# Kernel tuning notes

Measured on AMD Instinct MI355X. Metric: run time of the kernel, lower is better.

Reference implementation:

```python
import jax, jax.numpy as jnp
import numpy as np
import math

BS, SEQ, DIM, H, LK = 4, 4096, 768, 12, 256
HD = DIM // H  # 64
WIN = SEQ // LK  # 16, AdaptiveAvgPool1d reduces to uniform windows since SEQ % LK == 0


def setup_inputs() -> dict:
    key = jax.random.key(0)
    ks = jax.random.split(key, 12)
    s = 1.0 / math.sqrt(DIM)
    return {
        "query": jax.random.normal(ks[0], (BS, SEQ, DIM), jnp.float32),
        "key": jax.random.normal(ks[1], (BS, SEQ, DIM), jnp.float32),
        "value": jax.random.normal(ks[2], (BS, SEQ, DIM), jnp.float32),
        "mask": jax.random.normal(ks[3], (BS, SEQ), jnp.float32),  # mask<0 -> padded
        "Wq": jax.random.normal(ks[4], (DIM, DIM), jnp.float32) * s,
        "bq": jnp.zeros((DIM,), jnp.float32),
        "Wk": jax.random.normal(ks[5], (DIM, DIM), jnp.float32) * s,
        "bk": jnp.zeros((DIM,), jnp.float32),
        "Wv": jax.random.normal(ks[6], (DIM, DIM), jnp.float32) * s,
        "bv": jnp.zeros((DIM,), jnp.float32),
        "Wo": jax.random.normal(ks[7], (DIM, DIM), jnp.float32) * s,
        "bo": jnp.zeros((DIM,), jnp.float32),
    }


def reference(query, key, value, mask, Wq, bq, Wk, bk, Wv, bv, Wo, bo):
    bs, q_len, _ = query.shape
    # projections (nn.Linear: x @ W.T + b)
    Q = query @ Wq.T + bq
    K = key @ Wk.T + bk
    V = value @ Wv.T + bv
    # mask-fill padded K/V rows with 0 (mask dim==2 path: bool_mask = mask < 0)
    keep = (mask >= 0)[:, :, None]  # [bs, seq, 1]
    K = jnp.where(keep, K, 0.0)
    V = jnp.where(keep, V, 0.0)
    # adaptive avg pool over sequence -> linformer_k=256 (uniform windows of 16)
    Kc = K.reshape(bs, LK, WIN, DIM).mean(axis=2)  # [bs, 256, dim]
    Vc = V.reshape(bs, LK, WIN, DIM).mean(axis=2)
    # split heads
    Qh = Q.reshape(bs, q_len, H, HD) / math.sqrt(HD)  # scale fused
    Kh = Kc.reshape(bs, LK, H, HD)
    Vh = Vc.reshape(bs, LK, H, HD)
    # low-rank attention: [bs, h, q_len, 256]
    scores = jnp.einsum("bqhd,bkhd->bhqk", Qh, Kh)
    weights = jax.nn.softmax(scores, axis=-1)
    context = jnp.einsum("bhqk,bkhd->bqhd", weights, Vh).reshape(bs, q_len, DIM)
    return context @ Wo.T + bo
```

## Files before the change

kernel.cpp:

```cpp
#include <hip/hip_runtime.h>

#define BS_   4
#define SEQ_  4096
#define DIM_  768
#define NH_   12
#define HD_   64
#define LK_   256

typedef __attribute__((ext_vector_type(8))) short          bf8;
typedef __attribute__((ext_vector_type(8))) unsigned short us8;
typedef __attribute__((ext_vector_type(4))) unsigned short us4;
typedef __attribute__((ext_vector_type(4))) float          f32x4;
typedef __attribute__((ext_vector_type(4))) unsigned int   u32x4;

typedef unsigned int u32g __attribute__((address_space(1)));
typedef unsigned int u32l __attribute__((address_space(3)));

#define LOG2E 1.44269504088896340736f

__device__ __forceinline__ unsigned short f2bf(float f) {
  unsigned u = __builtin_bit_cast(unsigned, f);
  u += 0x7fffu + ((u >> 16) & 1u);
  return (unsigned short)(u >> 16);
}

__device__ __forceinline__ us8 cvt8(const float* __restrict__ p) {
  const float4 a = *(const float4*)p;
  const float4 b = *(const float4*)(p + 4);
  us8 r;
  r[0] = f2bf(a.x); r[1] = f2bf(a.y); r[2] = f2bf(a.z); r[3] = f2bf(a.w);
  r[4] = f2bf(b.x); r[5] = f2bf(b.y); r[6] = f2bf(b.z); r[7] = f2bf(b.w);
  return r;
}

__device__ __forceinline__ f32x4 max4(f32x4 a, f32x4 b) {
  f32x4 r;
  r[0] = fmaxf(a[0], b[0]); r[1] = fmaxf(a[1], b[1]);
  r[2] = fmaxf(a[2], b[2]); r[3] = fmaxf(a[3], b[3]);
  return r;
}

__device__ __forceinline__ float fexp2(float x) {
  float r; asm("v_exp_f32 %0, %1" : "=v"(r) : "v"(x)); return r;
}
__device__ __forceinline__ unsigned cvtpk(float lo, float hi) {
  unsigned r; asm("v_cvt_pk_bf16_f32 %0, %1, %2" : "=v"(r) : "v"(lo), "v"(hi));
  return r;
}

__global__ __launch_bounds__(384) void prep_kernel(
    const float* __restrict__ key, const float* __restrict__ value,
    const float* __restrict__ mask, const float* __restrict__ query,
    const float* __restrict__ Wq, const float* __restrict__ Wk,
    const float* __restrict__ Wv, const float* __restrict__ Wo,
    unsigned short* __restrict__ pk, unsigned short* __restrict__ pv,
    float* __restrict__ frac,
    unsigned short* __restrict__ Qbf, unsigned short* __restrict__ Wbf)
{
  const int bid = blockIdx.x;
  const int tid = threadIdx.x;
  if (bid < 1024) {
    const int b = bid >> 8;
    const int l = bid & 255;
    __shared__ float keep[16];
    __shared__ int   wlist[16];
    __shared__ float wwt[16];
    __shared__ int   nk4s;
    if (tid < 16) keep[tid] = (mask[b * SEQ_ + l * 16 + tid] >= 0.f) ? 1.f : 0.f;
    __syncthreads();
    if (tid == 0) {
      int n = 0; float cnt = 0.f;
      for (int w = 0; w < 16; ++w)
        if (keep[w] != 0.f) { wlist[n] = w; wwt[n] = 1.f; ++n; cnt += 1.f; }
      frac[b * LK_ + l] = cnt * (1.f / 16.f);
      const int n8 = (n + 7) & ~7;
      for (int i = n; i < n8; ++i) { wlist[i] = wlist[0]; wwt[i] = 0.f; }
      if (n == 0) for (int i = 0; i < 8; ++i) { wlist[i] = 0; wwt[i] = 0.f; }
      nk4s = (n == 0) ? 0 : n8;
    }
    __syncthreads();
    const int nk8 = nk4s;
    const int isV = tid >= 192;
    const int c = isV ? tid - 192 : tid;
    const float* src = isV ? value : key;
    const float* base = src + (size_t)(b * SEQ_ + l * 16) * DIM_ + c * 4;
    float4 acc = make_float4(0.f, 0.f, 0.f, 0.f);
    for (int i = 0; i < nk8; i += 8) {
      #pragma unroll
      for (int u = 0; u < 8; ++u) {
        const float4 v = *(const float4*)(base + (size_t)wlist[i + u] * DIM_);
        const float w = wwt[i + u];
        acc.x = fmaf(w, v.x, acc.x); acc.y = fmaf(w, v.y, acc.y);
        acc.z = fmaf(w, v.z, acc.z); acc.w = fmaf(w, v.w, acc.w);
      }
    }
    const float s = 1.f / 16.f;
    unsigned short* dst = isV ? pv : pk;
    us4 o4;
    o4[0] = f2bf(acc.x * s); o4[1] = f2bf(acc.y * s);
    o4[2] = f2bf(acc.z * s); o4[3] = f2bf(acc.w * s);
    *(us4*)(dst + (size_t)(b * LK_ + l) * DIM_ + c * 4) = o4;
    return;
  }
  const int QN8 = (BS_ * SEQ_ * DIM_) / 8;
  const int WN8 = (DIM_ * DIM_) / 8;
  const int i0 = (bid - 1024) * 768 + tid;
  #pragma unroll
  for (int u = 0; u < 2; ++u) {
    const int i = i0 + u * 384;
    if (i < QN8) { *(us8*)(Qbf + (size_t)i * 8) = cvt8(query + (size_t)i * 8); continue; }
    int j = i - QN8;
    const float* src; unsigned short* dst;
    if      (j <     WN8) { src = Wq; dst = Wbf;                   }
    else if (j < 2 * WN8) { src = Wk; dst = Wbf + DIM_*DIM_;     j -=     WN8; }
    else if (j < 3 * WN8) { src = Wv; dst = Wbf + 2*DIM_*DIM_;   j -= 2 * WN8; }
    else if (j < 4 * WN8) { src = Wo; dst = Wbf + 3*DIM_*DIM_;   j -= 3 * WN8; }
    else continue;
    *(us8*)(dst + (size_t)j * 8) = cvt8(src + (size_t)j * 8);
  }
}

template<int MODE, int SWZ>
__global__ __launch_bounds__(256) void gemm_bt(
    const void* __restrict__ Aptr_, const void* __restrict__ Bptr_,
    const float* __restrict__ bias, const float* __restrict__ bias2,
    const float* __restrict__ frac,
    void* __restrict__ Cout, float scale)
{
  constexpr int K  = DIM_;
  constexpr int BK = 64;
  constexpr int NT = K / BK;
  __shared__ __align__(16) unsigned short lA[2][128 * BK];
  __shared__ __align__(16) unsigned short lB[2][128 * BK];
  const int tid  = threadIdx.x;
  const int lane = tid & 63;
  const int wave = tid >> 6;

  int bx, by;
  if (SWZ) {
    const int r = (blockIdx.x & 7) * 96 + (blockIdx.x >> 3);
    bx = r / 6; by = r % 6;
  } else {
    bx = blockIdx.x; by = blockIdx.y;
  }
  const int brow = bx * 128;
  const int bcol = by * 128;

  const unsigned short* A  = (const unsigned short*)Aptr_;
  const unsigned short* Bw = (const unsigned short*)Bptr_;
  const float* bb = bias;
  int isV = 0;
  if (MODE == 34) {
    isV = blockIdx.z;
    A  += (size_t)isV * (BS_ * LK_ * DIM_);
    Bw += (size_t)isV * (DIM_ * DIM_);
    if (isV) bb = bias2;
  }

  const int wr = (wave >> 1) * 64;
  const int wc = (wave & 1) * 64;
  const int fr = lane & 15;
  const int hi = lane >> 4;
  const int rx = fr & 7;

  f32x4 acc[4][4];
  #pragma unroll
  for (int i = 0; i < 4; ++i)
    #pragma unroll
    for (int j = 0; j < 4; ++j) acc[i][j] = (f32x4){0.f, 0.f, 0.f, 0.f};

  const int srow = tid >> 3;
  const int schk = ((tid & 7) ^ (srow & 7)) * 8;

  auto STAGE = [&](int t, int b) {
    const int k0 = t * BK;
    #pragma unroll
    for (int s = 0; s < 4; ++s) {
      __builtin_amdgcn_global_load_lds(
          (const u32g*)(A + (size_t)(brow + srow + s * 32) * K + k0 + schk),
          (u32l*)&lA[b][s * 2048 + tid * 8], 16, 0, 0);
      __builtin_amdgcn_global_load_lds(
          (const u32g*)(Bw + (size_t)(bcol + srow + s * 32) * K + k0 + schk),
          (u32l*)&lB[b][s * 2048 + tid * 8], 16, 0, 0);
    }
  };

  auto COMPUTE = [&](int b) {
    #pragma unroll
    for (int ks = 0; ks < 2; ++ks) {
      bf8 af[4], bfv[4];
      const int c = ks * 4 + hi;
      const int pc = (c ^ rx) * 8;
      #pragma unroll
      for (int mi = 0; mi < 4; ++mi)
        af[mi] = *(const bf8*)&lA[b][(wr + mi * 16 + fr) * BK + pc];
      #pragma unroll
      for (int ni = 0; ni < 4; ++ni)
        bfv[ni] = *(const bf8*)&lB[b][(wc + ni * 16 + fr) * BK + pc];
      #pragma unroll
      for (int mi = 0; mi < 4; ++mi)
        #pragma unroll
        for (int ni = 0; ni < 4; ++ni)
          acc[mi][ni] = __builtin_amdgcn_mfma_f32_16x16x32_bf16(af[mi], bfv[ni], acc[mi][ni], 0, 0, 0);
    }
  };

  STAGE(0, 0);
  STAGE(1, 1);
  asm volatile("s_waitcnt vmcnt(8)" ::: "memory");
  __builtin_amdgcn_s_barrier();

  #pragma unroll 2
  for (int t = 0; t < NT; ++t) {
    COMPUTE(t & 1);
    if (t + 1 < NT) {
      __builtin_amdgcn_s_barrier();
      if (t + 2 < NT) {
        STAGE(t + 2, t & 1);
        asm volatile("s_waitcnt vmcnt(8)" ::: "memory");
      } else {
        asm volatile("s_waitcnt vmcnt(0)" ::: "memory");
      }
      __builtin_amdgcn_s_barrier();
    }
  }

  const int er = (lane >> 4) * 4;
  #pragma unroll
  for (int mi = 0; mi < 4; ++mi) {
    #pragma unroll
    for (int ni = 0; ni < 4; ++ni) {
      #pragma unroll
      for (int j = 0; j < 4; ++j) {
        const int r = brow + wr + mi * 16 + er + j;
        const int c = bcol + wc + ni * 16 + fr;
        float v = acc[mi][ni][j];
        if (MODE == 0) {
          v = (v + bias[c]) * scale;
          ((unsigned short*)Cout)[(size_t)r * DIM_ + c] = f2bf(v);
        } else if (MODE == 2) {
          ((float*)Cout)[(size_t)r * DIM_ + c] = v + bias[c];
        } else {
          v += frac[r] * bb[c];
          const int bb_ = r >> 8, key = r & 255;
          const int hh = c >> 6, dd = c & 63;
          const int bh = bb_ * NH_ + hh;
          size_t idx;
          if (isV) {
            idx = (size_t)bh * 16384 +
                ((key >> 5) * 4 + (dd >> 4)) * 512 + ((key >> 3) & 3) * 128 +
                (dd & 15) * 8 + (key & 7) + 786432;
          } else {
            const int tt = key >> 5, g = (key >> 3) & 3, sub = (key >> 2) & 1, jj = key & 3;
            const int frk = g * 4 + jj;
            idx = (size_t)bh * 16384 +
                (((tt * 2 + sub) * 2) + (dd >> 5)) * 512 + ((dd >> 3) & 3) * 128 +
                frk * 8 + (dd & 7);
          }
          ((unsigned short*)Cout)[idx] = f2bf(v);
        }
      }
    }
  }
}

__global__ __launch_bounds__(512, 4) void attn_fused(
    const unsigned short* __restrict__ Qh,
    const unsigned short* __restrict__ Kf,
    const unsigned short* __restrict__ Vf,
    unsigned short* __restrict__ ctx)
{
  __shared__ __align__(16) unsigned short Ks[16384];
  const int tid  = threadIdx.x;
  const int lane = tid & 63;
  const int wave = tid >> 6;
  const int bh = blockIdx.y;
  const int b = bh / NH_, h = bh % NH_;
  const int fr = lane & 15;
  const int hi = lane >> 4;
  const int qrow = blockIdx.x * 128 + wave * 16;

  {
    const unsigned short* kg = Kf + (size_t)bh * 16384 + tid * 8;
    #pragma unroll
    for (int i = 0; i < 4; ++i)
      __builtin_amdgcn_global_load_lds((const u32g*)(kg + i * 4096),
                                       (u32l*)&Ks[i * 4096 + tid * 8], 16, 0, 0);
  }

  const unsigned short* qp = Qh + (size_t)(b * SEQ_ + qrow + fr) * DIM_ + h * HD_ + hi * 8;
  const bf8 q0 = *(const bf8*)qp;
  const bf8 q1 = *(const bf8*)(qp + 32);

  __syncthreads();

  f32x4 scA[8], scB[8];
  __builtin_amdgcn_s_setprio(1);
  #pragma unroll
  for (int s = 0; s < 8; ++s) {
    const bf8 ka0 = *(const bf8*)&Ks[(s * 4 + 0) * 512 + lane * 8];
    const bf8 ka1 = *(const bf8*)&Ks[(s * 4 + 1) * 512 + lane * 8];
    const bf8 kb0 = *(const bf8*)&Ks[(s * 4 + 2) * 512 + lane * 8];
    const bf8 kb1 = *(const bf8*)&Ks[(s * 4 + 3) * 512 + lane * 8];
    f32x4 x = (f32x4){0.f, 0.f, 0.f, 0.f};
    x = __builtin_amdgcn_mfma_f32_16x16x32_bf16(ka0, q0, x, 0, 0, 0);
    x = __builtin_amdgcn_mfma_f32_16x16x32_bf16(ka1, q1, x, 0, 0, 0);
    scA[s] = x;
    f32x4 y = (f32x4){0.f, 0.f, 0.f, 0.f};
    y = __builtin_amdgcn_mfma_f32_16x16x32_bf16(kb0, q0, y, 0, 0, 0);
    y = __builtin_amdgcn_mfma_f32_16x16x32_bf16(kb1, q1, y, 0, 0, 0);
    scB[s] = y;
  }
  __builtin_amdgcn_s_setprio(0);

  f32x4 tm[8];
  #pragma unroll
  for (int s = 0; s < 8; ++s) tm[s] = max4(scA[s], scB[s]);
  tm[0] = max4(tm[0], tm[4]); tm[1] = max4(tm[1], tm[5]);
  tm[2] = max4(tm[2], tm[6]); tm[3] = max4(tm[3], tm[7]);
  tm[0] = max4(tm[0], tm[2]); tm[1] = max4(tm[1], tm[3]);
  tm[0] = max4(tm[0], tm[1]);
  float m = fmaxf(fmaxf(tm[0][0], tm[0][1]), fmaxf(tm[0][2], tm[0][3]));
  m = fmaxf(m, __shfl_xor(m, 16));
  m = fmaxf(m, __shfl_xor(m, 32));

  f32x4 uA = (f32x4){0.f, 0.f, 0.f, 0.f};
  f32x4 uB = (f32x4){0.f, 0.f, 0.f, 0.f};
  #pragma unroll
  for (int s = 0; s < 8; ++s) {
    #pragma unroll
    for (int j = 0; j < 4; ++j) {
      scA[s][j] = fexp2(scA[s][j] - m);
      scB[s][j] = fexp2(scB[s][j] - m);
    }
    uA += scA[s];
    uB += scB[s];
  }
  const f32x4 uv = uA + uB;
  float sum = (uv[0] + uv[1]) + (uv[2] + uv[3]);
  sum += __shfl_xor(sum, 16);
  sum += __shfl_xor(sum, 32);
  const float inv = 1.f / sum;

  bf8 pa[8];
  #pragma unroll
  for (int s = 0; s < 8; ++s) {
    u32x4 w;
    w[0] = cvtpk(scA[s][0] * inv, scA[s][1] * inv);
    w[1] = cvtpk(scA[s][2] * inv, scA[s][3] * inv);
    w[2] = cvtpk(scB[s][0] * inv, scB[s][1] * inv);
    w[3] = cvtpk(scB[s][2] * inv, scB[s][3] * inv);
    pa[s] = __builtin_bit_cast(bf8, w);
  }

  const unsigned short* vb = Vf + (size_t)bh * 16384 + lane * 8;
  f32x4 acc[4];
  #pragma unroll
  for (int ct = 0; ct < 4; ++ct) acc[ct] = (f32x4){0.f, 0.f, 0.f, 0.f};
  __builtin_amdgcn_s_setprio(1);
  #pragma unroll
  for (int s = 0; s < 8; ++s) {
    #pragma unroll
    for (int ct = 0; ct < 4; ++ct) {
      const bf8 vf = *(const bf8*)(vb + (s * 4 + ct) * 512);
      acc[ct] = __builtin_amdgcn_mfma_f32_16x16x32_bf16(pa[s], vf, acc[ct], 0, 0, 0);
    }
  }
  __builtin_amdgcn_s_setprio(0);

  #pragma unroll
  for (int ct = 0; ct < 4; ++ct)
    #pragma unroll
    for (int j = 0; j < 4; ++j)
      ctx[(size_t)(b * SEQ_ + qrow + hi * 4 + j) * DIM_ + h * HD_ + ct * 16 + fr] =
          f2bf(acc[ct][j]);
}

extern "C" void kernel_launch(void* const* d_in, const int* in_sizes, int n_in,
                              void* d_out, int out_size, void* d_ws, size_t ws_size,
                              hipStream_t stream) {
  const float* query = (const float*)d_in[0];
  const float* key   = (const float*)d_in[1];
  const float* value = (const float*)d_in[2];
  const float* mask  = (const float*)d_in[3];
  const float* Wq    = (const float*)d_in[4];
  const float* bq    = (const float*)d_in[5];
  const float* Wk    = (const float*)d_in[6];
  const float* bk    = (const float*)d_in[7];
  const float* Wv    = (const float*)d_in[8];
  const float* bv    = (const float*)d_in[9];
  const float* Wo    = (const float*)d_in[10];
  const float* bo    = (const float*)d_in[11];
  float* out = (float*)d_out;

  char* ws = (char*)d_ws;
  unsigned short* Qh  = (unsigned short*)ws;
  unsigned short* ctx = (unsigned short*)(ws + 25165824);
  unsigned short* pK  = (unsigned short*)(ws + 50331648);
  unsigned short* pV  = (unsigned short*)(ws + 51904512);
  unsigned short* Kf  = (unsigned short*)(ws + 53477376);
  unsigned short* Vf  = (unsigned short*)(ws + 55050240);
  float*          frac = (float*)(ws + 56623104);
  unsigned short* Wbf = (unsigned short*)(ws + 56627200);
  unsigned short* Qbf = ctx;

  const float qscale = 0.125f * LOG2E;

  prep_kernel<<<dim3(3456), dim3(384), 0, stream>>>(
      key, value, mask, query, Wq, Wk, Wv, Wo, pK, pV, frac, Qbf, Wbf);
  gemm_bt<0, 1><<<dim3(768), dim3(256), 0, stream>>>(
      Qbf, Wbf, bq, nullptr, nullptr, Qh, qscale);
  gemm_bt<34, 0><<<dim3(8, 6, 2), dim3(256), 0, stream>>>(
      pK, Wbf + DIM_*DIM_, bk, bv, frac, Kf, 1.f);
  attn_fused<<<dim3(32, 48), dim3(512), 0, stream>>>(Qh, Kf, Vf, ctx);
  gemm_bt<2, 1><<<dim3(768), dim3(256), 0, stream>>>(
      ctx, Wbf + 3*DIM_*DIM_, bo, nullptr, nullptr, out, 1.f);
}
```

Measured before the change: 127.2 us.

## Fuse fp32-to-bf16 query conversion into the Q projection GEMM

Removes the separate pass in the prep kernel that converted the full fp32 query tensor to bf16 and wrote it to the workspace. A new GEMM kernel loads fp32 query tiles straight into LDS and converts them to bf16 in registers just before the MFMA, using a 64x128 tile. This cuts one full read and write of the query activation tensor, but doubles the A-tile LDS footprint and adds conversion instructions to the GEMM inner loop, with smaller tiles and more blocks.

```diff
diff --git a/kernel.cpp b/kernel.cpp
--- a/kernel.cpp
+++ b/kernel.cpp
@@ -50,12 +50,11 @@
 
 __global__ __launch_bounds__(384) void prep_kernel(
     const float* __restrict__ key, const float* __restrict__ value,
-    const float* __restrict__ mask, const float* __restrict__ query,
+    const float* __restrict__ mask,
     const float* __restrict__ Wq, const float* __restrict__ Wk,
     const float* __restrict__ Wv, const float* __restrict__ Wo,
     unsigned short* __restrict__ pk, unsigned short* __restrict__ pv,
-    float* __restrict__ frac,
-    unsigned short* __restrict__ Qbf, unsigned short* __restrict__ Wbf)
+    float* __restrict__ frac, unsigned short* __restrict__ Wbf)
 {
   const int bid = blockIdx.x;
   const int tid = threadIdx.x;
@@ -102,14 +101,11 @@
     *(us4*)(dst + (size_t)(b * LK_ + l) * DIM_ + c * 4) = o4;
     return;
   }
-  const int QN8 = (BS_ * SEQ_ * DIM_) / 8;
   const int WN8 = (DIM_ * DIM_) / 8;
-  const int i0 = (bid - 1024) * 768 + tid;
-  #pragma unroll
-  for (int u = 0; u < 2; ++u) {
-    const int i = i0 + u * 384;
-    if (i < QN8) { *(us8*)(Qbf + (size_t)i * 8) = cvt8(query + (size_t)i * 8); continue; }
-    int j = i - QN8;
+  const int i0 = (bid - 1024) * 1536 + tid;
+  #pragma unroll
+  for (int u = 0; u < 4; ++u) {
+    int j = i0 + u * 384;
     const float* src; unsigned short* dst;
     if      (j <     WN8) { src = Wq; dst = Wbf;                   }
     else if (j < 2 * WN8) { src = Wk; dst = Wbf + DIM_*DIM_;     j -=     WN8; }
@@ -118,6 +114,117 @@
     else continue;
     *(us8*)(dst + (size_t)j * 8) = cvt8(src + (size_t)j * 8);
   }
+}
+
+__global__ __launch_bounds__(256) void gemm_qf32(
+    const float* __restrict__ Af, const unsigned short* __restrict__ Bw,
+    const float* __restrict__ bias, unsigned short* __restrict__ Cout,
+    float scale)
+{
+  constexpr int K  = DIM_;
+  constexpr int BK = 64;
+  constexpr int NT = K / BK;
+  __shared__ __align__(16) float          lA[2][64 * BK];
+  __shared__ __align__(16) unsigned short lB[2][128 * BK];
+  const int tid  = threadIdx.x;
+  const int lane = tid & 63;
+  const int wave = tid >> 6;
+
+  const int r = (blockIdx.x & 7) * 192 + (blockIdx.x >> 3);
+  const int brow = (r / 6) * 64;
+  const int bcol = (r % 6) * 128;
+
+  const int wr = (wave >> 1) * 32;
+  const int wc = (wave & 1) * 64;
+  const int fr = lane & 15;
+  const int hi = lane >> 4;
+  const int rx = fr & 7;
+
+  f32x4 acc[2][4];
+  #pragma unroll
+  for (int i = 0; i < 2; ++i)
+    #pragma unroll
+    for (int j = 0; j < 4; ++j) acc[i][j] = (f32x4){0.f, 0.f, 0.f, 0.f};
+
+  const int srowB = tid >> 3;
+  const int schkB = ((tid & 7) ^ (srowB & 7)) * 8;
+  const int srowA = tid >> 4;
+  const int posA  = tid & 15;
+  const int csA   = ((posA >> 1) ^ (srowA & 7)) * 8 + (posA & 1) * 4;
+
+  auto STAGE = [&](int t, int b) {
+    const int k0 = t * BK;
+    #pragma unroll
+    for (int s = 0; s < 4; ++s) {
+      __builtin_amdgcn_global_load_lds(
+          (const u32g*)(Af + (size_t)(brow + s * 16 + srowA) * K + k0 + csA),
+          (u32l*)&lA[b][s * 1024 + tid * 4], 16, 0, 0);
+      __builtin_amdgcn_global_load_lds(
+          (const u32g*)(Bw + (size_t)(bcol + s * 32 + srowB) * K + k0 + schkB),
+          (u32l*)&lB[b][s * 2048 + tid * 8], 16, 0, 0);
+    }
+  };
+
+  auto COMPUTE = [&](int b) {
+    #pragma unroll
+    for (int ks = 0; ks < 2; ++ks) {
+      const int c  = ks * 4 + hi;
+      const int pc = c ^ rx;
+      bf8 af[2], bfv[4];
+      #pragma unroll
+      for (int mi = 0; mi < 2; ++mi) {
+        const int ro = (wr + mi * 16 + fr) * BK + pc * 8;
+        const f32x4 lo = *(const f32x4*)&lA[b][ro];
+        const f32x4 hi4 = *(const f32x4*)&lA[b][ro + 4];
+        u32x4 w;
+        w[0] = cvtpk(lo[0], lo[1]);
+        w[1] = cvtpk(lo[2], lo[3]);
+        w[2] = cvtpk(hi4[0], hi4[1]);
+        w[3] = cvtpk(hi4[2], hi4[3]);
+        af[mi] = __builtin_bit_cast(bf8, w);
+      }
+      #pragma unroll
+      for (int ni = 0; ni < 4; ++ni)
+        bfv[ni] = *(const bf8*)&lB[b][(wc + ni * 16 + fr) * BK + pc * 8];
+      #pragma unroll
+      for (int mi = 0; mi < 2; ++mi)
+        #pragma unroll
+        for (int ni = 0; ni < 4; ++ni)
+          acc[mi][ni] = __builtin_amdgcn_mfma_f32_16x16x32_bf16(af[mi], bfv[ni], acc[mi][ni], 0, 0, 0);
+    }
+  };
+
+  STAGE(0, 0);
+  STAGE(1, 1);
+  asm volatile("s_waitcnt vmcnt(8)" ::: "memory");
+  __builtin_amdgcn_s_barrier();
+
+  #pragma unroll 2
+  for (int t = 0; t < NT; ++t) {
+    COMPUTE(t & 1);
+    if (t + 1 < NT) {
+      __builtin_amdgcn_s_barrier();
+      if (t + 2 < NT) {
+        STAGE(t + 2, t & 1);
+        asm volatile("s_waitcnt vmcnt(8)" ::: "memory");
+      } else {
+        asm volatile("s_waitcnt vmcnt(0)" ::: "memory");
+      }
+      __builtin_amdgcn_s_barrier();
+    }
+  }
+
+  const int er = (lane >> 4) * 4;
+  #pragma unroll
+  for (int mi = 0; mi < 2; ++mi)
+    #pragma unroll
+    for (int ni = 0; ni < 4; ++ni)
+      #pragma unroll
+      for (int j = 0; j < 4; ++j) {
+        const int rr = brow + wr + mi * 16 + er + j;
+        const int cc = bcol + wc + ni * 16 + fr;
+        Cout[(size_t)rr * DIM_ + cc] = f2bf((acc[mi][ni][j] + bias[cc]) * scale);
+      }
 }
 
 template<int MODE, int SWZ>
@@ -235,10 +342,7 @@
         const int r = brow + wr + mi * 16 + er + j;
         const int c = bcol + wc + ni * 16 + fr;
         float v = acc[mi][ni][j];
-        if (MODE == 0) {
-          v = (v + bias[c]) * scale;
-          ((unsigned short*)Cout)[(size_t)r * DIM_ + c] = f2bf(v);
-        } else if (MODE == 2) {
+        if (MODE == 2) {
           ((float*)Cout)[(size_t)r * DIM_ + c] = v + bias[c];
         } else {
           v += frac[r] * bb[c];
@@ -402,14 +506,13 @@
   unsigned short* Vf  = (unsigned short*)(ws + 55050240);
   float*          frac = (float*)(ws + 56623104);
   unsigned short* Wbf = (unsigned short*)(ws + 56627200);
-  unsigned short* Qbf = ctx;
 
   const float qscale = 0.125f * LOG2E;
 
-  prep_kernel<<<dim3(3456), dim3(384), 0, stream>>>(
-      key, value, mask, query, Wq, Wk, Wv, Wo, pK, pV, frac, Qbf, Wbf);
-  gemm_bt<0, 1><<<dim3(768), dim3(256), 0, stream>>>(
-      Qbf, Wbf, bq, nullptr, nullptr, Qh, qscale);
+  prep_kernel<<<dim3(1216), dim3(384), 0, stream>>>(
+      key, value, mask, Wq, Wk, Wv, Wo, pK, pV, frac, Wbf);
+  gemm_qf32<<<dim3(1536), dim3(256), 0, stream>>>(
+      query, Wbf, bq, Qh, qscale);
   gemm_bt<34, 0><<<dim3(8, 6, 2), dim3(256), 0, stream>>>(
       pK, Wbf + DIM_*DIM_, bk, bv, frac, Kf, 1.f);
   attn_fused<<<dim3(32, 48), dim3(512), 0, stream>>>(Qh, Kf, Vf, ctx);
```

After: 128.5 us. No clear change (+1.0%).
